# Kernel optimization log

Hardware: AMD Instinct MI355X
Metric: run time of the kernel (lower is better)

The kernel has to match this reference:

```python
import jax, jax.numpy as jnp
import numpy as np


def setup_inputs() -> dict:
    key = jax.random.key(0)
    k1, k2 = jax.random.split(key)
    N, D, G = 1048576, 128, 1024
    features = jax.random.normal(k1, (N, D), dtype=jnp.float32)
    # sorted node->graph assignment, equivalent to torch.split by batch_num_nodes
    segment_ids = jnp.sort(jax.random.randint(k2, (N,), 0, G, dtype=jnp.int32))
    return {"features": features, "segment_ids": segment_ids, "num_graphs": G}


def reference(features, segment_ids, num_graphs):
    # Single fused segment-sum pass: sums node features per graph and stacks
    # into [num_graphs, d_feat], same math as split + per-chunk torch.sum + stack.
    return jax.ops.segment_sum(
        features, segment_ids, num_segments=num_graphs, indices_are_sorted=True
    )
```

## Files before the change

### kernel.cpp

```cpp
#include <hip/hip_runtime.h>
#include <hip/hip_bf16.h>


__global__ __launch_bounds__(256) void SumPooling_54700703482382_kernel(
    const float4* __restrict__ feat,
    const int*    __restrict__ seg,
    float4*       __restrict__ out,
    int N) {
    const int g = blockIdx.x;

    int lo = 0, hi = N;
    while (lo < hi) {
        int mid = (lo + hi) >> 1;
        if (seg[mid] < g) lo = mid + 1; else hi = mid;
    }
    const int start = lo;
    hi = N;
    while (lo < hi) {
        int mid = (lo + hi) >> 1;
        if (seg[mid] < g + 1) lo = mid + 1; else hi = mid;
    }
    const int end = lo;

    const int tid   = threadIdx.x;
    const int c     = tid & 31;
    const int rlane = tid >> 5;

    float4 acc = make_float4(0.f, 0.f, 0.f, 0.f);
    #pragma unroll 4
    for (int r = start + rlane; r < end; r += 8) {
        float4 v = feat[(size_t)r * 32 + c];
        acc.x += v.x; acc.y += v.y; acc.z += v.z; acc.w += v.w;
    }

    __shared__ float4 red[256];
    red[tid] = acc;
    __syncthreads();
    if (tid < 128) {
        float4 o = red[tid + 128];
        red[tid].x += o.x; red[tid].y += o.y; red[tid].z += o.z; red[tid].w += o.w;
    }
    __syncthreads();
    if (tid < 64) {
        float4 o = red[tid + 64];
        red[tid].x += o.x; red[tid].y += o.y; red[tid].z += o.z; red[tid].w += o.w;
    }
    __syncthreads();
    if (tid < 32) {
        float4 o = red[tid + 32];
        float4 r0 = red[tid];
        r0.x += o.x; r0.y += o.y; r0.z += o.z; r0.w += o.w;
        out[(size_t)g * 32 + tid] = r0;
    }
}

extern "C" void kernel_launch(void* const* d_in, const int* in_sizes, int n_in,
                              void* d_out, int out_size, void* d_ws, size_t ws_size,
                              hipStream_t stream) {
    const float4* feat = (const float4*)d_in[0];
    const int*    seg  = (const int*)d_in[1];
    float4*       out  = (float4*)d_out;

    const int N = in_sizes[1];
    const int D = in_sizes[0] / N;
    const int G = out_size / D;

    SumPooling_54700703482382_kernel<<<G, 256, 0, stream>>>(feat, seg, out, N);
}
```

Baseline: 109.0 us.

## Precompute segment offsets in a pre-pass and use nontemporal vector loads

Adds a boundary kernel that writes per-graph start offsets into workspace, which replaces the two binary searches each block ran over the segment id array. The main loop now walks a precomputed pointer with an exact iteration count, unrolled 8, and reads features with nontemporal loads. The cost is an extra kernel launch that reads all segment ids. The loop is bandwidth-bound on about 512MB of features, so the search removal and load hints are expected to matter only a little.

```diff
diff --git a/kernel.cpp b/kernel.cpp
--- a/kernel.cpp
+++ b/kernel.cpp
@@ -2,54 +2,52 @@
 #include <hip/hip_bf16.h>
 
 
+typedef float v4f __attribute__((ext_vector_type(4)));
+
+__global__ __launch_bounds__(256) void seg_boundaries_kernel(
+    const int* __restrict__ seg, int* __restrict__ offs, int N, int G) {
+    int i = blockIdx.x * blockDim.x + threadIdx.x;
+    if (i >= N) return;
+    int s = seg[i];
+    int prev = (i == 0) ? -1 : seg[i - 1];
+    for (int g = prev + 1; g <= s; ++g) offs[g] = i;
+    if (i == N - 1) {
+        for (int g = s + 1; g <= G; ++g) offs[g] = N;
+    }
+}
+
 __global__ __launch_bounds__(256) void SumPooling_54700703482382_kernel(
-    const float4* __restrict__ feat,
-    const int*    __restrict__ seg,
-    float4*       __restrict__ out,
-    int N) {
-    const int g = blockIdx.x;
-
-    int lo = 0, hi = N;
-    while (lo < hi) {
-        int mid = (lo + hi) >> 1;
-        if (seg[mid] < g) lo = mid + 1; else hi = mid;
-    }
-    const int start = lo;
-    hi = N;
-    while (lo < hi) {
-        int mid = (lo + hi) >> 1;
-        if (seg[mid] < g + 1) lo = mid + 1; else hi = mid;
-    }
-    const int end = lo;
+    const v4f* __restrict__ feat,
+    const int* __restrict__ offs,
+    v4f*       __restrict__ out) {
+    const int g     = blockIdx.x;
+    const int start = offs[g];
+    const int end   = offs[g + 1];
 
     const int tid   = threadIdx.x;
     const int c     = tid & 31;
     const int rlane = tid >> 5;
 
-    float4 acc = make_float4(0.f, 0.f, 0.f, 0.f);
-    #pragma unroll 4
-    for (int r = start + rlane; r < end; r += 8) {
-        float4 v = feat[(size_t)r * 32 + c];
-        acc.x += v.x; acc.y += v.y; acc.z += v.z; acc.w += v.w;
+    v4f acc = (v4f)(0.f);
+    const v4f* p = feat + (size_t)start * 32 + (size_t)rlane * 32 + c;
+    int iters = (end - start - rlane + 7) >> 3;
+
+    #pragma unroll 8
+    for (int it = 0; it < iters; ++it) {
+        v4f v = __builtin_nontemporal_load(p);
+        acc += v;
+        p += 8 * 32;
     }
 
-    __shared__ float4 red[256];
+    __shared__ v4f red[256];
     red[tid] = acc;
     __syncthreads();
-    if (tid < 128) {
-        float4 o = red[tid + 128];
-        red[tid].x += o.x; red[tid].y += o.y; red[tid].z += o.z; red[tid].w += o.w;
-    }
+    if (tid < 128) red[tid] += red[tid + 128];
     __syncthreads();
-    if (tid < 64) {
-        float4 o = red[tid + 64];
-        red[tid].x += o.x; red[tid].y += o.y; red[tid].z += o.z; red[tid].w += o.w;
-    }
+    if (tid < 64) red[tid] += red[tid + 64];
     __syncthreads();
     if (tid < 32) {
-        float4 o = red[tid + 32];
-        float4 r0 = red[tid];
-        r0.x += o.x; r0.y += o.y; r0.z += o.z; r0.w += o.w;
+        v4f r0 = red[tid] + red[tid + 32];
         out[(size_t)g * 32 + tid] = r0;
     }
 }
@@ -57,13 +55,16 @@
 extern "C" void kernel_launch(void* const* d_in, const int* in_sizes, int n_in,
                               void* d_out, int out_size, void* d_ws, size_t ws_size,
                               hipStream_t stream) {
-    const float4* feat = (const float4*)d_in[0];
-    const int*    seg  = (const int*)d_in[1];
-    float4*       out  = (float4*)d_out;
+    const v4f* feat = (const v4f*)d_in[0];
+    const int* seg  = (const int*)d_in[1];
+    v4f*       out  = (v4f*)d_out;
 
     const int N = in_sizes[1];
     const int D = in_sizes[0] / N;
     const int G = out_size / D;
 
-    SumPooling_54700703482382_kernel<<<G, 256, 0, stream>>>(feat, seg, out, N);
+    int* offs = (int*)d_ws;
+
+    seg_boundaries_kernel<<<(N + 255) / 256, 256, 0, stream>>>(seg, offs, N, G);
+    SumPooling_54700703482382_kernel<<<G, 256, 0, stream>>>(feat, offs, out);
 }
```

Result: faster. 91.33 us (-16.2%).
